# Optimization experiments

Hardware: AMD Instinct MI355X
Metric: run time of the kernel (lower is better)

Reference implementation:

```python
import jax, jax.numpy as jnp
import numpy as np

N = 50000   # nodes
E = 640000  # edges (before self-loops)
D = 128     # in_dim == out_dim
H = 4       # heads
C = 32      # per-head channels (out_dim // heads)
ED = 1      # edge_dim
NEG_SLOPE = 0.2
LN_EPS = 1e-5


def setup_inputs() -> dict:
    key = jax.random.key(0)
    ks = jax.random.split(key, 8)
    glorot = lambda k, sh, fan: jax.random.normal(k, sh, jnp.float32) / np.float32(np.sqrt(fan))
    return dict(
        x=jax.random.normal(ks[0], (N, D), jnp.float32),
        edge_index=jax.random.randint(ks[1], (2, E), 0, N, dtype=jnp.int32),
        edge_attr=jax.random.uniform(ks[2], (E, ED), jnp.float32),
        W_l=glorot(ks[3], (D, H * C), D), b_l=jnp.zeros((H * C,), jnp.float32),
        W_r=glorot(ks[4], (D, H * C), D), b_r=jnp.zeros((H * C,), jnp.float32),
        W_e=glorot(ks[5], (ED, H * C), ED),
        att=glorot(ks[6], (H, C), C),
        bias=jnp.zeros((H * C,), jnp.float32),
        ln_gamma=jnp.ones((H * C,), jnp.float32),
        ln_beta=jnp.zeros((H * C,), jnp.float32),
    )


def reference(x, edge_index, edge_attr, W_l, b_l, W_r, b_r, W_e, att, bias, ln_gamma, ln_beta):
    n = x.shape[0]
    src, dst = edge_index[0], edge_index[1]
    # --- add self loops; self-loop edge_attr = mean of incoming attrs (PyG fill_value='mean') ---
    attr_sum = jax.ops.segment_sum(edge_attr, dst, num_segments=n)          # (N, ED)
    cnt = jax.ops.segment_sum(jnp.ones((edge_attr.shape[0], 1), edge_attr.dtype), dst, num_segments=n)
    loop_attr = attr_sum / jnp.maximum(cnt, 1.0)
    ea = jnp.concatenate([edge_attr, loop_attr], axis=0)                    # (E+N, ED)
    loop = jnp.arange(n, dtype=src.dtype)
    src = jnp.concatenate([src, loop])
    dst = jnp.concatenate([dst, loop])
    # --- GATv2: separate source/target linear transforms ---
    x_l = (x @ W_l + b_l).reshape(n, H, C)   # source (x_j)
    x_r = (x @ W_r + b_r).reshape(n, H, C)   # target (x_i)
    e_f = (ea @ W_e).reshape(-1, H, C)       # edge embedding (E+N, H, C)
    xj = x_l[src]                            # gather (E+N, H, C)
    m = jax.nn.leaky_relu(xj + x_r[dst] + e_f, NEG_SLOPE)
    alpha = jnp.einsum('ehc,hc->eh', m, att)
    # --- segment softmax over incoming edges of each target node ---
    amax = jax.ops.segment_max(alpha, dst, num_segments=n)  # every node has a self-loop
    ex = jnp.exp(alpha - amax[dst])
    denom = jax.ops.segment_sum(ex, dst, num_segments=n)
    a = ex / denom[dst]                                     # (E+N, H); attn dropout is eval no-op
    # --- scatter-aggregate messages, concat heads, conv bias ---
    out = jax.ops.segment_sum(xj * a[..., None], dst, num_segments=n).reshape(n, H * C) + bias
    # --- ELU, dropout (eval no-op), residual (in_dim == out_dim, no res_proj), LayerNorm ---
    out = jax.nn.elu(out) + x
    mu = jnp.mean(out, axis=-1, keepdims=True)
    var = jnp.var(out, axis=-1, keepdims=True)
    return (out - mu) * jax.lax.rsqrt(var + LN_EPS) * ln_gamma + ln_beta
```

## Files before the change

### kernel.cpp

```cpp
#include <hip/hip_runtime.h>
#include <hip/hip_fp16.h>
#include <math.h>

#define DCH 128
#define NEG 0.2f
#define LOG2E 1.44269504088896f
#define NPART 256
#define SCAP 20
#define BCAP 1152

typedef _Float16 f16x8 __attribute__((ext_vector_type(8)));
typedef float    f32x4 __attribute__((ext_vector_type(4)));
typedef float    f32x2 __attribute__((ext_vector_type(2)));
typedef unsigned long long u64;

static __device__ __forceinline__ float dpp_radd16(float v) {
    int b;
    b = __builtin_amdgcn_update_dpp(0, __float_as_int(v), 0xB1, 0xF, 0xF, true);
    v += __int_as_float(b);
    b = __builtin_amdgcn_update_dpp(0, __float_as_int(v), 0x4E, 0xF, 0xF, true);
    v += __int_as_float(b);
    b = __builtin_amdgcn_update_dpp(0, __float_as_int(v), 0x141, 0xF, 0xF, true);
    v += __int_as_float(b);
    b = __builtin_amdgcn_update_dpp(0, __float_as_int(v), 0x140, 0xF, 0xF, true);
    v += __int_as_float(b);
    return v;
}

__global__ __launch_bounds__(256) void k_prep(
        const float* __restrict__ x, __half* __restrict__ xf16, int total4,
        const float* __restrict__ Wl, const float* __restrict__ Wr,
        __half* __restrict__ wtl, __half* __restrict__ wtr, int nb_cvt) {
    int bid = blockIdx.x;
    if (bid < nb_cvt) {
        int i = bid * 256 + (int)threadIdx.x;
        if (i >= total4) return;
        float4 v = ((const float4*)x)[i];
        __half2* dst = (__half2*)xf16 + 2 * (size_t)i;
        dst[0] = __floats2half2_rn(v.x, v.y);
        dst[1] = __floats2half2_rn(v.z, v.w);
    } else {
        int t = (bid - nb_cvt) * 256 + (int)threadIdx.x;
        if (t >= 2 * DCH * DCH) return;
        const float* W = (t < DCH * DCH) ? Wl : Wr;
        __half* wt = (t < DCH * DCH) ? wtl : wtr;
        int u = t & (DCH * DCH - 1);
        int k = u >> 7, j = u & 127;
        wt[j * 128 + k] = __float2half_rn(W[u]);
    }
}

__global__ __launch_bounds__(256) void k_mmpart(
        const __half* __restrict__ xf16,
        const __half* __restrict__ wtl, const __half* __restrict__ wtr,
        const float* __restrict__ bl, const float* __restrict__ br,
        __half* __restrict__ xl16, float* __restrict__ xro, int N,
        const int* __restrict__ ei, const float* __restrict__ eattr,
        unsigned* __restrict__ sorted, unsigned* __restrict__ cnt,
        int E, int NB, int chunkE, int nb_mm) {
    if ((int)blockIdx.x >= nb_mm) {
        __shared__ unsigned cur[1024];
        int p = (int)blockIdx.x - nb_mm;
        for (int i = threadIdx.x; i < 1024; i += 256) cur[i] = 0u;
        __syncthreads();
        int e0 = p * chunkE;
        int e1 = e0 + chunkE; if (e1 > E) e1 = E;
        for (int e = e0 + (int)threadIdx.x; e < e1; e += 256) {
            int d = ei[E + e], s = ei[e];
            float a = eattr[e];
            int b = d >> 6, dl = d & 63;
            unsigned q = (unsigned)fminf(a * 1024.f + 0.5f, 1023.f);
            unsigned rank = atomicAdd(&cur[b], 1u);
            if (rank < SCAP)
                sorted[((size_t)b * NPART + p) * SCAP + rank] =
                    (unsigned)dl | ((unsigned)s << 6) | (q << 22);
        }
        __syncthreads();
        for (int b = threadIdx.x; b < NB; b += 256) {
            unsigned c = cur[b];
            cnt[(size_t)b * NPART + p] = c < SCAP ? c : SCAP;
        }
        return;
    }
    int wave = threadIdx.x >> 6, lane = threadIdx.x & 63;
    int node0 = blockIdx.x * 64;
    int jbase = wave * 32;
    int rl = lane & 15, kg = lane >> 4;
    f32x4 acc[4][2][2];
    #pragma unroll
    for (int a = 0; a < 4; ++a)
        #pragma unroll
        for (int b = 0; b < 2; ++b)
            #pragma unroll
            for (int c = 0; c < 2; ++c)
                acc[a][b][c] = (f32x4){0.f, 0.f, 0.f, 0.f};
    #pragma unroll
    for (int ks = 0; ks < 4; ++ks) {
        int koff = ks * 32 + kg * 8;
        f16x8 av[4];
        #pragma unroll
        for (int rt = 0; rt < 4; ++rt) {
            int row = node0 + rt * 16 + rl;
            if (row >= N) row = N - 1;
            av[rt] = *(const f16x8*)(xf16 + (size_t)row * 128 + koff);
        }
        #pragma unroll
        for (int jt = 0; jt < 2; ++jt) {
            int j = jbase + jt * 16 + rl;
            size_t ob = (size_t)j * 128 + koff;
            f16x8 bL = *(const f16x8*)(wtl + ob);
            f16x8 bR = *(const f16x8*)(wtr + ob);
            #pragma unroll
            for (int rt = 0; rt < 4; ++rt) {
                acc[rt][jt][0] = __builtin_amdgcn_mfma_f32_16x16x32_f16(av[rt], bL, acc[rt][jt][0], 0, 0, 0);
                acc[rt][jt][1] = __builtin_amdgcn_mfma_f32_16x16x32_f16(av[rt], bR, acc[rt][jt][1], 0, 0, 0);
            }
        }
    }
    float blv[2], brv[2];
    #pragma unroll
    for (int jt = 0; jt < 2; ++jt) {
        int j = jbase + jt * 16 + rl;
        blv[jt] = bl[j]; brv[jt] = br[j];
    }
    #pragma unroll
    for (int rt = 0; rt < 4; ++rt) {
        #pragma unroll
        for (int r = 0; r < 4; ++r) {
            int row = node0 + rt * 16 + kg * 4 + r;
            if (row < N) {
                #pragma unroll
                for (int jt = 0; jt < 2; ++jt) {
                    int j = jbase + jt * 16 + rl;
                    xl16[(size_t)row * 128 + j] = __float2half_rn(acc[rt][jt][0][r] + blv[jt]);
                    xro[(size_t)row * 128 + j] = acc[rt][jt][1][r] + brv[jt];
                }
            }
        }
    }
}

__global__ __launch_bounds__(256) void k_fill2(
        const unsigned* __restrict__ sorted, const unsigned* __restrict__ cnt,
        unsigned* __restrict__ csr, uint2* __restrict__ ndesc,
        float* __restrict__ lattr, int N) {
    __shared__ unsigned lraw[BCAP];
    __shared__ unsigned hcnt[64], qsum[64];
    __shared__ unsigned wsum[4], wpre[5];
    __shared__ int ncur[64];
    __shared__ int tot_s;
    int t = threadIdx.x, lane = t & 63, w = t >> 6;
    int bucket = blockIdx.x;
    if (t < 64) { hcnt[t] = 0u; qsum[t] = 0u; }
    unsigned v = cnt[(size_t)bucket * NPART + t];
    int sc = (int)v;
    #pragma unroll
    for (int o = 1; o < 64; o <<= 1) {
        int tmp = __shfl_up(sc, o, 64);
        if (lane >= o) sc += tmp;
    }
    if (lane == 63) wsum[w] = (unsigned)sc;
    __syncthreads();
    if (t == 0) {
        wpre[0] = 0;
        #pragma unroll
        for (int k = 0; k < 4; ++k) wpre[k + 1] = wpre[k] + wsum[k];
        tot_s = (int)(wpre[4] < BCAP ? wpre[4] : BCAP);
    }
    __syncthreads();
    unsigned sb = wpre[w] + (unsigned)sc - v;
    {
        const unsigned* src = sorted + ((size_t)bucket * NPART + t) * SCAP;
        for (int i = 0; i < (int)v; ++i) {
            unsigned idx = sb + (unsigned)i;
            if (idx < BCAP) {
                unsigned rec = src[i];
                lraw[idx] = rec;
                int dl = (int)(rec & 63u);
                atomicAdd(&hcnt[dl], 1u);
                atomicAdd(&qsum[dl], rec >> 22);
            }
        }
    }
    __syncthreads();
    if (t < 64) {
        int nv = (int)hcnt[t], nsc = nv;
        #pragma unroll
        for (int o = 1; o < 64; o <<= 1) {
            int tmp = __shfl_up(nsc, o, 64);
            if (t >= o) nsc += tmp;
        }
        int nb = nsc - nv;
        ncur[t] = nb;
        int node = bucket * 64 + t;
        if (node < N) {
            ndesc[node] = make_uint2((unsigned)(bucket * BCAP + nb), (unsigned)nv);
            lattr[node] = ((float)qsum[t] * (1.f / 1024.f)) / fmaxf((float)nv, 1.f);
        }
    }
    __syncthreads();
    int tot = tot_s;
    for (int i = t; i < tot; i += 256) {
        unsigned rec = lraw[i];
        int dl = (int)(rec & 63u);
        int pos = atomicAdd(&ncur[dl], 1);
        csr[(size_t)bucket * BCAP + pos] = ((rec >> 6) & 0xFFFFu) | ((rec >> 22) << 16);
    }
}

__global__ __launch_bounds__(256) void k_gat(
        const __half* __restrict__ xl16, const float* __restrict__ xrp, const float* __restrict__ x,
        const unsigned* __restrict__ csr, const uint2* __restrict__ ndesc,
        const float* __restrict__ lattr,
        const float* __restrict__ We, const float* __restrict__ att, const float* __restrict__ bias,
        const float* __restrict__ gamma, const float* __restrict__ beta,
        float* __restrict__ out, int N) {
    int wid = threadIdx.x >> 6;
    int lane = threadIdx.x & 63;
    int node = blockIdx.x * 4 + wid;
    if (node >= N) return;
    int c0 = lane << 1;
    const __half2* xlh = (const __half2*)xl16;
    f32x2 xrv = ((const f32x2*)xrp)[(size_t)node * 64 + lane];
    f32x2 att2 = { att[c0] * LOG2E, att[c0 + 1] * LOG2E };
    f32x2 we2  = { We[c0], We[c0 + 1] };
    uint2 nd = ndesc[node];
    float la = lattr[node];
    int beg = (int)nd.x, end = (int)(nd.x + nd.y);
    f32x2 accA = {0.f, 0.f}, accB = {0.f, 0.f}, accC = {0.f, 0.f}, accD = {0.f, 0.f};
    float den0 = 0.f, den1 = 0.f, den2 = 0.f, den3 = 0.f;

    auto upd = [&](float& den, f32x2& acc, float ea, __half2 hv) {
        float2 gf = __half22float2(hv);
        f32x2 g = { gf.x, gf.y };
        f32x2 tv = g + (xrv + ea * we2);
        f32x2 tn = tv * NEG;
        tv.x = fmaxf(tv.x, tn.x);
        tv.y = fmaxf(tv.y, tn.y);
        float pt = tv.x * att2.x + tv.y * att2.y;
        pt = dpp_radd16(pt);
        float pe = exp2f(pt);
        den += pe;
        acc += pe * g;
    };

    upd(den1, accB, la, xlh[(size_t)node * 64 + lane]);

    int p = beg;
    unsigned e0 = 0, e1 = 0, e2 = 0, e3 = 0;
    bool have = (p + 4 <= end);
    if (have) { e0 = csr[p]; e1 = csr[p + 1]; e2 = csr[p + 2]; e3 = csr[p + 3]; }
    while (have) {
        __half2 g0 = xlh[(size_t)(e0 & 0xFFFFu) * 64 + lane];
        __half2 g1 = xlh[(size_t)(e1 & 0xFFFFu) * 64 + lane];
        __half2 g2 = xlh[(size_t)(e2 & 0xFFFFu) * 64 + lane];
        __half2 g3 = xlh[(size_t)(e3 & 0xFFFFu) * 64 + lane];
        int np = p + 4;
        bool nhave = (np + 4 <= end);
        unsigned f0 = 0, f1 = 0, f2 = 0, f3 = 0;
        if (nhave) { f0 = csr[np]; f1 = csr[np + 1]; f2 = csr[np + 2]; f3 = csr[np + 3]; }
        upd(den0, accA, (float)(e0 >> 16) * (1.f / 1024.f), g0);
        upd(den1, accB, (float)(e1 >> 16) * (1.f / 1024.f), g1);
        upd(den2, accC, (float)(e2 >> 16) * (1.f / 1024.f), g2);
        upd(den3, accD, (float)(e3 >> 16) * (1.f / 1024.f), g3);
        p = np;
        e0 = f0; e1 = f1; e2 = f2; e3 = f3;
        have = nhave;
    }
    while (p < end) {
        unsigned e = csr[p];
        __half2 g = xlh[(size_t)(e & 0xFFFFu) * 64 + lane];
        upd(den0, accA, (float)(e >> 16) * (1.f / 1024.f), g);
        ++p;
    }

    float denom = (den0 + den1) + (den2 + den3);
    f32x2 acc = (accA + accB) + (accC + accD);
    float inv = 1.f / denom;
    float o0 = acc.x * inv + bias[c0];
    float o1 = acc.y * inv + bias[c0 + 1];
    o0 = o0 > 0.f ? o0 : (__expf(o0) - 1.f);
    o1 = o1 > 0.f ? o1 : (__expf(o1) - 1.f);
    f32x2 xv = ((const f32x2*)x)[(size_t)node * 64 + lane];
    o0 += xv.x; o1 += xv.y;
    float r1 = o0 + o1, r2 = o0 * o0 + o1 * o1;
    #pragma unroll
    for (int mk = 1; mk < 64; mk <<= 1) {
        r1 += __shfl_xor(r1, mk, 64);
        r2 += __shfl_xor(r2, mk, 64);
    }
    float mean = r1 * (1.f / 128.f);
    float var  = r2 * (1.f / 128.f) - mean * mean;
    float rr = rsqrtf(var + 1e-5f);
    float2 ov;
    ov.x = (o0 - mean) * rr * gamma[c0]     + beta[c0];
    ov.y = (o1 - mean) * rr * gamma[c0 + 1] + beta[c0 + 1];
    ((float2*)out)[(size_t)node * 64 + lane] = ov;
}

extern "C" void kernel_launch(void* const* d_in, const int* in_sizes, int n_in,
                              void* d_out, int out_size, void* d_ws, size_t ws_size,
                              hipStream_t stream) {
    const float* x     = (const float*)d_in[0];
    const int*   ei    = (const int*)d_in[1];
    const float* eattr = (const float*)d_in[2];
    const float* Wl    = (const float*)d_in[3];
    const float* bl    = (const float*)d_in[4];
    const float* Wr    = (const float*)d_in[5];
    const float* br    = (const float*)d_in[6];
    const float* We    = (const float*)d_in[7];
    const float* att   = (const float*)d_in[8];
    const float* bias  = (const float*)d_in[9];
    const float* gam   = (const float*)d_in[10];
    const float* bet   = (const float*)d_in[11];
    float* out = (float*)d_out;
    int N = in_sizes[0] / DCH;
    int E = in_sizes[1] / 2;
    int NB = (N + 63) / 64;

    char* base = (char*)d_ws;
    size_t off = 0;
    auto alloc = [&](size_t nbytes) -> void* {
        void* p = base + off;
        off += (nbytes + 255) & ~(size_t)255;
        return p;
    };
    unsigned* sorted = (unsigned*)alloc((size_t)NB * NPART * SCAP * 4);
    unsigned* cnt    = (unsigned*)alloc((size_t)NB * NPART * 4);
    unsigned* csr    = (unsigned*)alloc((size_t)NB * BCAP * 4);
    uint2*    ndesc  = (uint2*)alloc((size_t)N * 8);
    float*    lattr  = (float*)alloc((size_t)N * 4);
    __half*   xl16   = (__half*)alloc((size_t)N * DCH * 2);
    float*    xrb    = (float*)alloc((size_t)N * DCH * 4);
    __half*   xf16   = (__half*)alloc((size_t)N * DCH * 2);
    __half*   wtl    = (__half*)alloc((size_t)DCH * DCH * 2);
    __half*   wtr    = (__half*)alloc((size_t)DCH * DCH * 2);
    (void)n_in; (void)out_size; (void)ws_size;

    int total4  = N * DCH / 4;
    int nb_cvt  = (total4 + 255) / 256;
    int nb_cvtw = (2 * DCH * DCH + 255) / 256;
    int nb_mm   = (N + 63) / 64;
    int chunkE  = (E + NPART - 1) / NPART;

    k_prep<<<nb_cvt + nb_cvtw, 256, 0, stream>>>(
        x, xf16, total4, Wl, Wr, wtl, wtr, nb_cvt);
    k_mmpart<<<nb_mm + NPART, 256, 0, stream>>>(
        xf16, wtl, wtr, bl, br, xl16, xrb, N,
        ei, eattr, sorted, cnt, E, NB, chunkE, nb_mm);
    k_fill2<<<NB, 256, 0, stream>>>(
        sorted, cnt, csr, ndesc, lattr, N);
    k_gat<<<(N + 3) / 4, 256, 0, stream>>>(
        xl16, xrb, x, csr, ndesc, lattr, We, att, bias, gam, bet, out, N);
}
```

Baseline: 97.76 us.

## Split wave into four edge groups with 8 channels per lane in GAT aggregation

Restructures the per-node aggregation kernel so each 64-lane wave handles four edges at once. Each 16-lane quarter takes its own edge, and each lane loads 8 fp16 channels with a 16-byte vector load instead of 2 channels per lane. The per-head dot product now reduces over 4 lanes instead of 16, and partial sums are merged across quarters with cross-lane shuffles at the end. This is meant to cut loop iterations and widen memory transactions per gather, at the cost of masked work on the tail iteration and extra shuffle reductions.

```diff
diff --git a/kernel.cpp b/kernel.cpp
--- a/kernel.cpp
+++ b/kernel.cpp
@@ -14,15 +14,11 @@
 typedef float    f32x2 __attribute__((ext_vector_type(2)));
 typedef unsigned long long u64;
 
-static __device__ __forceinline__ float dpp_radd16(float v) {
+static __device__ __forceinline__ float dpp_radd4(float v) {
     int b;
     b = __builtin_amdgcn_update_dpp(0, __float_as_int(v), 0xB1, 0xF, 0xF, true);
     v += __int_as_float(b);
     b = __builtin_amdgcn_update_dpp(0, __float_as_int(v), 0x4E, 0xF, 0xF, true);
-    v += __int_as_float(b);
-    b = __builtin_amdgcn_update_dpp(0, __float_as_int(v), 0x141, 0xF, 0xF, true);
-    v += __int_as_float(b);
-    b = __builtin_amdgcn_update_dpp(0, __float_as_int(v), 0x140, 0xF, 0xF, true);
     v += __int_as_float(b);
     return v;
 }
@@ -219,83 +215,121 @@
     int lane = threadIdx.x & 63;
     int node = blockIdx.x * 4 + wid;
     if (node >= N) return;
-    int c0 = lane << 1;
-    const __half2* xlh = (const __half2*)xl16;
-    f32x2 xrv = ((const f32x2*)xrp)[(size_t)node * 64 + lane];
-    f32x2 att2 = { att[c0] * LOG2E, att[c0 + 1] * LOG2E };
-    f32x2 we2  = { We[c0], We[c0 + 1] };
+    int q = lane >> 4;
+    int sl = lane & 15;
+    int c8 = sl << 3;
+
+    float4 attA = *(const float4*)(att + c8);
+    float4 attB = *(const float4*)(att + c8 + 4);
+    attA.x *= LOG2E; attA.y *= LOG2E; attA.z *= LOG2E; attA.w *= LOG2E;
+    attB.x *= LOG2E; attB.y *= LOG2E; attB.z *= LOG2E; attB.w *= LOG2E;
+    float4 weA = *(const float4*)(We + c8);
+    float4 weB = *(const float4*)(We + c8 + 4);
+    float4 xrA = *(const float4*)(xrp + (size_t)node * 128 + c8);
+    float4 xrB = *(const float4*)(xrp + (size_t)node * 128 + c8 + 4);
+
     uint2 nd = ndesc[node];
+    int beg = (int)nd.x, deg = (int)nd.y;
     float la = lattr[node];
-    int beg = (int)nd.x, end = (int)(nd.x + nd.y);
-    f32x2 accA = {0.f, 0.f}, accB = {0.f, 0.f}, accC = {0.f, 0.f}, accD = {0.f, 0.f};
-    float den0 = 0.f, den1 = 0.f, den2 = 0.f, den3 = 0.f;
-
-    auto upd = [&](float& den, f32x2& acc, float ea, __half2 hv) {
-        float2 gf = __half22float2(hv);
-        f32x2 g = { gf.x, gf.y };
-        f32x2 tv = g + (xrv + ea * we2);
-        f32x2 tn = tv * NEG;
-        tv.x = fmaxf(tv.x, tn.x);
-        tv.y = fmaxf(tv.y, tn.y);
-        float pt = tv.x * att2.x + tv.y * att2.y;
-        pt = dpp_radd16(pt);
-        float pe = exp2f(pt);
+    int T = deg + 1;
+
+    float4 accA = {0.f, 0.f, 0.f, 0.f}, accB = {0.f, 0.f, 0.f, 0.f};
+    float den = 0.f;
+
+    for (int p = 0; p < T; p += 4) {
+        int idx = p + q;
+        bool isReal = idx < deg;
+        unsigned rec = 0u;
+        if (isReal) rec = csr[beg + idx];
+        int src = isReal ? (int)(rec & 0xFFFFu) : node;
+        float ea = isReal ? (float)(rec >> 16) * (1.f / 1024.f) : la;
+        float vmask = (idx <= deg) ? 1.f : 0.f;
+        uint4 graw = *(const uint4*)(xl16 + ((size_t)src << 7) + c8);
+        float2 g0 = __half22float2(*(const __half2*)&graw.x);
+        float2 g1 = __half22float2(*(const __half2*)&graw.y);
+        float2 g2 = __half22float2(*(const __half2*)&graw.z);
+        float2 g3 = __half22float2(*(const __half2*)&graw.w);
+        float t0 = g0.x + fmaf(ea, weA.x, xrA.x); t0 = fmaxf(t0, t0 * NEG);
+        float t1 = g0.y + fmaf(ea, weA.y, xrA.y); t1 = fmaxf(t1, t1 * NEG);
+        float t2 = g1.x + fmaf(ea, weA.z, xrA.z); t2 = fmaxf(t2, t2 * NEG);
+        float t3 = g1.y + fmaf(ea, weA.w, xrA.w); t3 = fmaxf(t3, t3 * NEG);
+        float t4 = g2.x + fmaf(ea, weB.x, xrB.x); t4 = fmaxf(t4, t4 * NEG);
+        float t5 = g2.y + fmaf(ea, weB.y, xrB.y); t5 = fmaxf(t5, t5 * NEG);
+        float t6 = g3.x + fmaf(ea, weB.z, xrB.z); t6 = fmaxf(t6, t6 * NEG);
+        float t7 = g3.y + fmaf(ea, weB.w, xrB.w); t7 = fmaxf(t7, t7 * NEG);
+        float d = t0 * attA.x;
+        d = fmaf(t1, attA.y, d); d = fmaf(t2, attA.z, d); d = fmaf(t3, attA.w, d);
+        d = fmaf(t4, attB.x, d); d = fmaf(t5, attB.y, d); d = fmaf(t6, attB.z, d);
+        d = fmaf(t7, attB.w, d);
+        float pt = dpp_radd4(d);
+        float pe = exp2f(pt) * vmask;
         den += pe;
-        acc += pe * g;
-    };
-
-    upd(den1, accB, la, xlh[(size_t)node * 64 + lane]);
-
-    int p = beg;
-    unsigned e0 = 0, e1 = 0, e2 = 0, e3 = 0;
-    bool have = (p + 4 <= end);
-    if (have) { e0 = csr[p]; e1 = csr[p + 1]; e2 = csr[p + 2]; e3 = csr[p + 3]; }
-    while (have) {
-        __half2 g0 = xlh[(size_t)(e0 & 0xFFFFu) * 64 + lane];
-        __half2 g1 = xlh[(size_t)(e1 & 0xFFFFu) * 64 + lane];
-        __half2 g2 = xlh[(size_t)(e2 & 0xFFFFu) * 64 + lane];
-        __half2 g3 = xlh[(size_t)(e3 & 0xFFFFu) * 64 + lane];
-        int np = p + 4;
-        bool nhave = (np + 4 <= end);
-        unsigned f0 = 0, f1 = 0, f2 = 0, f3 = 0;
-        if (nhave) { f0 = csr[np]; f1 = csr[np + 1]; f2 = csr[np + 2]; f3 = csr[np + 3]; }
-        upd(den0, accA, (float)(e0 >> 16) * (1.f / 1024.f), g0);
-        upd(den1, accB, (float)(e1 >> 16) * (1.f / 1024.f), g1);
-        upd(den2, accC, (float)(e2 >> 16) * (1.f / 1024.f), g2);
-        upd(den3, accD, (float)(e3 >> 16) * (1.f / 1024.f), g3);
-        p = np;
-        e0 = f0; e1 = f1; e2 = f2; e3 = f3;
-        have = nhave;
-    }
-    while (p < end) {
-        unsigned e = csr[p];
-        __half2 g = xlh[(size_t)(e & 0xFFFFu) * 64 + lane];
-        upd(den0, accA, (float)(e >> 16) * (1.f / 1024.f), g);
-        ++p;
-    }
-
-    float denom = (den0 + den1) + (den2 + den3);
-    f32x2 acc = (accA + accB) + (accC + accD);
-    float inv = 1.f / denom;
-    float o0 = acc.x * inv + bias[c0];
-    float o1 = acc.y * inv + bias[c0 + 1];
+        accA.x = fmaf(pe, g0.x, accA.x); accA.y = fmaf(pe, g0.y, accA.y);
+        accA.z = fmaf(pe, g1.x, accA.z); accA.w = fmaf(pe, g1.y, accA.w);
+        accB.x = fmaf(pe, g2.x, accB.x); accB.y = fmaf(pe, g2.y, accB.y);
+        accB.z = fmaf(pe, g3.x, accB.z); accB.w = fmaf(pe, g3.y, accB.w);
+    }
+
+    den += __shfl_xor(den, 16, 64);
+    accA.x += __shfl_xor(accA.x, 16, 64); accA.y += __shfl_xor(accA.y, 16, 64);
+    accA.z += __shfl_xor(accA.z, 16, 64); accA.w += __shfl_xor(accA.w, 16, 64);
+    accB.x += __shfl_xor(accB.x, 16, 64); accB.y += __shfl_xor(accB.y, 16, 64);
+    accB.z += __shfl_xor(accB.z, 16, 64); accB.w += __shfl_xor(accB.w, 16, 64);
+    den += __shfl_xor(den, 32, 64);
+    accA.x += __shfl_xor(accA.x, 32, 64); accA.y += __shfl_xor(accA.y, 32, 64);
+    accA.z += __shfl_xor(accA.z, 32, 64); accA.w += __shfl_xor(accA.w, 32, 64);
+    accB.x += __shfl_xor(accB.x, 32, 64); accB.y += __shfl_xor(accB.y, 32, 64);
+    accB.z += __shfl_xor(accB.z, 32, 64); accB.w += __shfl_xor(accB.w, 32, 64);
+
+    float inv = 1.f / den;
+    float4 biA = *(const float4*)(bias + c8);
+    float4 biB = *(const float4*)(bias + c8 + 4);
+    float o0 = fmaf(accA.x, inv, biA.x), o1 = fmaf(accA.y, inv, biA.y);
+    float o2 = fmaf(accA.z, inv, biA.z), o3 = fmaf(accA.w, inv, biA.w);
+    float o4 = fmaf(accB.x, inv, biB.x), o5 = fmaf(accB.y, inv, biB.y);
+    float o6 = fmaf(accB.z, inv, biB.z), o7 = fmaf(accB.w, inv, biB.w);
     o0 = o0 > 0.f ? o0 : (__expf(o0) - 1.f);
     o1 = o1 > 0.f ? o1 : (__expf(o1) - 1.f);
-    f32x2 xv = ((const f32x2*)x)[(size_t)node * 64 + lane];
-    o0 += xv.x; o1 += xv.y;
-    float r1 = o0 + o1, r2 = o0 * o0 + o1 * o1;
-    #pragma unroll
-    for (int mk = 1; mk < 64; mk <<= 1) {
-        r1 += __shfl_xor(r1, mk, 64);
-        r2 += __shfl_xor(r2, mk, 64);
+    o2 = o2 > 0.f ? o2 : (__expf(o2) - 1.f);
+    o3 = o3 > 0.f ? o3 : (__expf(o3) - 1.f);
+    o4 = o4 > 0.f ? o4 : (__expf(o4) - 1.f);
+    o5 = o5 > 0.f ? o5 : (__expf(o5) - 1.f);
+    o6 = o6 > 0.f ? o6 : (__expf(o6) - 1.f);
+    o7 = o7 > 0.f ? o7 : (__expf(o7) - 1.f);
+    float4 xvA = *(const float4*)(x + (size_t)node * 128 + c8);
+    float4 xvB = *(const float4*)(x + (size_t)node * 128 + c8 + 4);
+    o0 += xvA.x; o1 += xvA.y; o2 += xvA.z; o3 += xvA.w;
+    o4 += xvB.x; o5 += xvB.y; o6 += xvB.z; o7 += xvB.w;
+    float r1 = ((o0 + o1) + (o2 + o3)) + ((o4 + o5) + (o6 + o7));
+    float r2 = o0 * o0;
+    r2 = fmaf(o1, o1, r2); r2 = fmaf(o2, o2, r2); r2 = fmaf(o3, o3, r2);
+    r2 = fmaf(o4, o4, r2); r2 = fmaf(o5, o5, r2); r2 = fmaf(o6, o6, r2);
+    r2 = fmaf(o7, o7, r2);
+    #pragma unroll
+    for (int mk = 1; mk < 16; mk <<= 1) {
+        r1 += __shfl_xor(r1, mk, 16);
+        r2 += __shfl_xor(r2, mk, 16);
     }
     float mean = r1 * (1.f / 128.f);
     float var  = r2 * (1.f / 128.f) - mean * mean;
     float rr = rsqrtf(var + 1e-5f);
-    float2 ov;
-    ov.x = (o0 - mean) * rr * gamma[c0]     + beta[c0];
-    ov.y = (o1 - mean) * rr * gamma[c0 + 1] + beta[c0 + 1];
-    ((float2*)out)[(size_t)node * 64 + lane] = ov;
+    if (q == 0) {
+        float4 gmA = *(const float4*)(gamma + c8);
+        float4 gmB = *(const float4*)(gamma + c8 + 4);
+        float4 btA = *(const float4*)(beta + c8);
+        float4 btB = *(const float4*)(beta + c8 + 4);
+        float4 wA, wB;
+        wA.x = (o0 - mean) * rr * gmA.x + btA.x;
+        wA.y = (o1 - mean) * rr * gmA.y + btA.y;
+        wA.z = (o2 - mean) * rr * gmA.z + btA.z;
+        wA.w = (o3 - mean) * rr * gmA.w + btA.w;
+        wB.x = (o4 - mean) * rr * gmB.x + btB.x;
+        wB.y = (o5 - mean) * rr * gmB.y + btB.y;
+        wB.z = (o6 - mean) * rr * gmB.z + btB.z;
+        wB.w = (o7 - mean) * rr * gmB.w + btB.w;
+        *(float4*)(out + (size_t)node * 128 + c8) = wA;
+        *(float4*)(out + (size_t)node * 128 + c8 + 4) = wB;
+    }
 }
 
 extern "C" void kernel_launch(void* const* d_in, const int* in_sizes, int n_in,
```

Result: no change. 98.76 us (+1.0%).
